# Optimization experiments

Hardware: AMD Instinct MI355X
Metric: run time of the kernel (lower is better)

The kernel has to match this reference:

```python
import jax, jax.numpy as jnp
import numpy as np

SIZE = 128
RATIO = 0.5

def setup_inputs() -> dict:
    key = jax.random.key(0)
    k1, k2, k3 = jax.random.split(key, 3)
    B, D, K = 16, 256, 18
    assp_features = jax.random.normal(k1, (B, D, SIZE, SIZE), dtype=jnp.float32)
    prototypes = jax.random.normal(k2, (B, K, D), dtype=jnp.float32)
    n_samp = int(SIZE * SIZE * RATIO)
    # sample without replacement, matching np.random.choice(replace=False)
    random_indices = jax.random.permutation(k3, SIZE * SIZE)[:n_samp].astype(jnp.int64)
    return {"assp_features": assp_features, "prototypes": prototypes,
            "random_indices": random_indices}

def reference(assp_features, prototypes, random_indices):
    # assp_features: [B, D, H, W], prototypes: [B, K, D], random_indices: [N]
    size = assp_features.shape[-1]
    x = random_indices // size  # [N]
    y = random_indices % size   # [N]
    f = assp_features[:, :, x, y]            # [B, D, N] gathered pixel features
    # squared L2 distances [B, N, K]; argmin of ||p-f||_2 == argmin of squared dist
    p2 = jnp.sum(prototypes * prototypes, axis=-1)       # [B, K]
    f2 = jnp.sum(f * f, axis=1)                          # [B, N]
    cross = jnp.einsum('bdn,bkd->bnk', f, prototypes)    # [B, N, K]
    d2 = p2[:, None, :] - 2.0 * cross + f2[:, :, None]
    idx = jnp.argmin(d2, axis=-1)                        # [B, N]
    nearest = jnp.take_along_axis(prototypes, idx[..., None], axis=1)  # [B, N, D]
    out = assp_features.at[:, :, x, y].set(jnp.swapaxes(nearest, 1, 2))
    return out
```

## Files before the change

kernel.cpp:

```cpp
#include <hip/hip_runtime.h>

constexpr int B = 16;
constexpr int D = 256;
constexpr int K = 18;
constexpr int SZ = 128;
constexpr int S = SZ * SZ;
constexpr int N = S / 2;
constexpr int PB = 512;

__global__ __launch_bounds__(256) void prep_kernel(
    const float* __restrict__ proto,
    const int* __restrict__ idx,
    unsigned char* __restrict__ mask,
    double* __restrict__ p2,
    double* __restrict__ p64,
    float* __restrict__ pT32) {
  const int blk = blockIdx.x;
  if (blk < 32) {
    mask[idx[blk * 256 + threadIdx.x]] = 1;
  } else if (blk < 104) {
    const int row  = (blk - 32) * 4 + (threadIdx.x >> 6);
    const int lane = threadIdx.x & 63;
    const float4 v = *(const float4*)(proto + (size_t)row * D + lane * 4);
    double s = (double)v.x * (double)v.x + (double)v.y * (double)v.y
             + (double)v.z * (double)v.z + (double)v.w * (double)v.w;
#pragma unroll
    for (int off = 1; off < 64; off <<= 1)
      s += __shfl_xor(s, off, 64);
    if (lane == 0) p2[row] = s;
  } else {
    const int e = (blk - 104) * 256 + threadIdx.x;
    const int b = e / (D * K);
    const int r = e - b * (D * K);
    const int d = r / K;
    const int k = r - d * K;
    const float v = proto[((size_t)b * K + k) * D + d];
    p64[e]  = (double)v;
    pT32[e] = v;
  }
}

__global__ __launch_bounds__(128, 2) void fused_kernel(
    const float* __restrict__ assp,
    const double* __restrict__ p64,
    const float* __restrict__ pT32,
    const double* __restrict__ p2,
    const unsigned char* __restrict__ mask,
    float* __restrict__ out) {
  __shared__ double spd[D * K];

  const int b     = blockIdx.x & 15;
  const int chunk = blockIdx.x >> 4;
  const int pos0  = chunk * PB;
  const int tid   = threadIdx.x;

  const double* pb = p64 + (size_t)b * D * K;
  for (int i = tid; i < D * K; i += 128) spd[i] = pb[i];
  __syncthreads();

  const float* fin = assp + (size_t)(b * D) * S + pos0 + 2 * tid;

  double acc[4][K];
#pragma unroll
  for (int jp = 0; jp < 4; ++jp)
#pragma unroll
    for (int k = 0; k < K; ++k) acc[jp][k] = 0.0;

  for (int d0 = 0; d0 < D; d0 += 8) {
    float2 fv[8][2];
#pragma unroll
    for (int jd = 0; jd < 8; ++jd) {
      fv[jd][0] = *(const float2*)(fin + (size_t)(d0 + jd) * S);
      fv[jd][1] = *(const float2*)(fin + (size_t)(d0 + jd) * S + 256);
    }
#pragma unroll
    for (int jd = 0; jd < 8; ++jd) {
      const double f0 = (double)fv[jd][0].x;
      const double f1 = (double)fv[jd][0].y;
      const double f2 = (double)fv[jd][1].x;
      const double f3 = (double)fv[jd][1].y;
      const double* pr = &spd[(d0 + jd) * K];
#pragma unroll
      for (int k = 0; k < K; ++k) {
        const double pk = pr[k];
        acc[0][k] += f0 * pk;
        acc[1][k] += f1 * pk;
        acc[2][k] += f2 * pk;
        acc[3][k] += f3 * pk;
      }
    }
  }

  const double* p2b = p2 + b * K;
  double best[4];
  int kst[4];
#pragma unroll
  for (int jp = 0; jp < 4; ++jp) { best[jp] = 1e300; kst[jp] = 0; }
#pragma unroll
  for (int k = 0; k < K; ++k) {
    const double pk2 = p2b[k];
#pragma unroll
    for (int jp = 0; jp < 4; ++jp) {
      const double d2 = pk2 - 2.0 * acc[jp][k];
      if (d2 < best[jp]) { best[jp] = d2; kst[jp] = k; }
    }
  }

  const uchar2 m0 = *(const uchar2*)(mask + pos0 + 2 * tid);
  const uchar2 m1 = *(const uchar2*)(mask + pos0 + 256 + 2 * tid);
  const float* pt = pT32 + (size_t)b * D * K;
  float* op = out + (size_t)(b * D) * S + pos0 + 2 * tid;

  for (int d0 = 0; d0 < D; d0 += 8) {
#pragma unroll
    for (int jd = 0; jd < 8; ++jd) {
      const int d = d0 + jd;
      const float2 fa = *(const float2*)(fin + (size_t)d * S);
      const float2 fb = *(const float2*)(fin + (size_t)d * S + 256);
      const float* prow = pt + d * K;
      float2 oa, ob;
      oa.x = m0.x ? prow[kst[0]] : fa.x;
      oa.y = m0.y ? prow[kst[1]] : fa.y;
      ob.x = m1.x ? prow[kst[2]] : fb.x;
      ob.y = m1.y ? prow[kst[3]] : fb.y;
      *(float2*)(op + (size_t)d * S) = oa;
      *(float2*)(op + (size_t)d * S + 256) = ob;
    }
  }
}

extern "C" void kernel_launch(void* const* d_in, const int* in_sizes, int n_in,
                              void* d_out, int out_size, void* d_ws, size_t ws_size,
                              hipStream_t stream) {
  const float* assp  = (const float*)d_in[0];
  const float* proto = (const float*)d_in[1];
  const int*   idx   = (const int*)d_in[2];
  float* out = (float*)d_out;

  unsigned char* mask = (unsigned char*)d_ws;
  double*        p2   = (double*)((char*)d_ws + S);
  double*        p64  = (double*)((char*)d_ws + S + (size_t)B * K * 8);
  float*         pT32 = (float*)((char*)p64 + (size_t)B * D * K * 8);

  hipMemsetAsync(mask, 0, S, stream);
  prep_kernel<<<392, 256, 0, stream>>>(proto, idx, mask, p2, p64, pT32);
  fused_kernel<<<B * (S / PB), 128, 0, stream>>>(assp, p64, pT32, p2, mask, out);
}
```

Measured before the change: 229.9 us.

## Drop shared-memory prototype staging, use 256 threads with two pixels each

The fused kernel no longer copies the double-precision prototypes into LDS. It reads them directly from global memory through a padded 24-double stride, so every thread loads the same row and the access is uniform. Block size doubles to 256 threads with two pixels per thread instead of four, which halves the accumulator registers. The aim is higher occupancy and removing the 36KB LDS stage and its sync. The second pass also walks d in reverse, so it likely re-reads recently cached feature rows, and it prefetches the prototype values. The cost is that all prototype reads now go through global memory and cache instead of LDS.

```diff
diff --git a/kernel.cpp b/kernel.cpp
--- a/kernel.cpp
+++ b/kernel.cpp
@@ -6,6 +6,7 @@
 constexpr int SZ = 128;
 constexpr int S = SZ * SZ;
 constexpr int N = S / 2;
+constexpr int PSTR = 24;
 constexpr int PB = 512;
 
 __global__ __launch_bounds__(256) void prep_kernel(
@@ -35,96 +36,83 @@
     const int d = r / K;
     const int k = r - d * K;
     const float v = proto[((size_t)b * K + k) * D + d];
-    p64[e]  = (double)v;
-    pT32[e] = v;
+    p64[((size_t)b * D + d) * PSTR + k] = (double)v;
+    pT32[((size_t)b * D + d) * K + k]   = v;
   }
 }
 
-__global__ __launch_bounds__(128, 2) void fused_kernel(
+__global__ __launch_bounds__(256, 2) void fused_kernel(
     const float* __restrict__ assp,
     const double* __restrict__ p64,
     const float* __restrict__ pT32,
     const double* __restrict__ p2,
     const unsigned char* __restrict__ mask,
     float* __restrict__ out) {
-  __shared__ double spd[D * K];
-
   const int b     = blockIdx.x & 15;
   const int chunk = blockIdx.x >> 4;
   const int pos0  = chunk * PB;
   const int tid   = threadIdx.x;
 
-  const double* pb = p64 + (size_t)b * D * K;
-  for (int i = tid; i < D * K; i += 128) spd[i] = pb[i];
-  __syncthreads();
+  const float*  fin = assp + (size_t)(b * D) * S + pos0 + 2 * tid;
+  const double* pb  = p64 + (size_t)b * D * PSTR;
 
-  const float* fin = assp + (size_t)(b * D) * S + pos0 + 2 * tid;
-
-  double acc[4][K];
+  double acc0[K], acc1[K];
 #pragma unroll
-  for (int jp = 0; jp < 4; ++jp)
-#pragma unroll
-    for (int k = 0; k < K; ++k) acc[jp][k] = 0.0;
+  for (int k = 0; k < K; ++k) { acc0[k] = 0.0; acc1[k] = 0.0; }
 
   for (int d0 = 0; d0 < D; d0 += 8) {
-    float2 fv[8][2];
+    float2 fv[8];
+#pragma unroll
+    for (int jd = 0; jd < 8; ++jd)
+      fv[jd] = *(const float2*)(fin + (size_t)(d0 + jd) * S);
 #pragma unroll
     for (int jd = 0; jd < 8; ++jd) {
-      fv[jd][0] = *(const float2*)(fin + (size_t)(d0 + jd) * S);
-      fv[jd][1] = *(const float2*)(fin + (size_t)(d0 + jd) * S + 256);
-    }
-#pragma unroll
-    for (int jd = 0; jd < 8; ++jd) {
-      const double f0 = (double)fv[jd][0].x;
-      const double f1 = (double)fv[jd][0].y;
-      const double f2 = (double)fv[jd][1].x;
-      const double f3 = (double)fv[jd][1].y;
-      const double* pr = &spd[(d0 + jd) * K];
+      const double f0 = (double)fv[jd].x;
+      const double f1 = (double)fv[jd].y;
+      const double* pr = pb + (size_t)(d0 + jd) * PSTR;
 #pragma unroll
       for (int k = 0; k < K; ++k) {
         const double pk = pr[k];
-        acc[0][k] += f0 * pk;
-        acc[1][k] += f1 * pk;
-        acc[2][k] += f2 * pk;
-        acc[3][k] += f3 * pk;
+        acc0[k] += f0 * pk;
+        acc1[k] += f1 * pk;
       }
     }
   }
 
   const double* p2b = p2 + b * K;
-  double best[4];
-  int kst[4];
-#pragma unroll
-  for (int jp = 0; jp < 4; ++jp) { best[jp] = 1e300; kst[jp] = 0; }
+  double best0 = 1e300, best1 = 1e300;
+  int kst0 = 0, kst1 = 0;
 #pragma unroll
   for (int k = 0; k < K; ++k) {
     const double pk2 = p2b[k];
-#pragma unroll
-    for (int jp = 0; jp < 4; ++jp) {
-      const double d2 = pk2 - 2.0 * acc[jp][k];
-      if (d2 < best[jp]) { best[jp] = d2; kst[jp] = k; }
-    }
+    const double d20 = pk2 - 2.0 * acc0[k];
+    const double d21 = pk2 - 2.0 * acc1[k];
+    if (d20 < best0) { best0 = d20; kst0 = k; }
+    if (d21 < best1) { best1 = d21; kst1 = k; }
   }
 
-  const uchar2 m0 = *(const uchar2*)(mask + pos0 + 2 * tid);
-  const uchar2 m1 = *(const uchar2*)(mask + pos0 + 256 + 2 * tid);
-  const float* pt = pT32 + (size_t)b * D * K;
+  const uchar2 m = *(const uchar2*)(mask + pos0 + 2 * tid);
+  const float* g0 = pT32 + (size_t)b * D * K + kst0;
+  const float* g1 = pT32 + (size_t)b * D * K + kst1;
   float* op = out + (size_t)(b * D) * S + pos0 + 2 * tid;
 
-  for (int d0 = 0; d0 < D; d0 += 8) {
+  for (int d0 = D - 8; d0 >= 0; d0 -= 8) {
+    float2 fa[8];
+    float  pa[8], pbv[8];
 #pragma unroll
     for (int jd = 0; jd < 8; ++jd) {
       const int d = d0 + jd;
-      const float2 fa = *(const float2*)(fin + (size_t)d * S);
-      const float2 fb = *(const float2*)(fin + (size_t)d * S + 256);
-      const float* prow = pt + d * K;
-      float2 oa, ob;
-      oa.x = m0.x ? prow[kst[0]] : fa.x;
-      oa.y = m0.y ? prow[kst[1]] : fa.y;
-      ob.x = m1.x ? prow[kst[2]] : fb.x;
-      ob.y = m1.y ? prow[kst[3]] : fb.y;
-      *(float2*)(op + (size_t)d * S) = oa;
-      *(float2*)(op + (size_t)d * S + 256) = ob;
+      fa[jd]  = *(const float2*)(fin + (size_t)d * S);
+      pa[jd]  = g0[(size_t)d * K];
+      pbv[jd] = g1[(size_t)d * K];
+    }
+#pragma unroll
+    for (int jd = 0; jd < 8; ++jd) {
+      const int d = d0 + jd;
+      float2 o;
+      o.x = m.x ? pa[jd]  : fa[jd].x;
+      o.y = m.y ? pbv[jd] : fa[jd].y;
+      *(float2*)(op + (size_t)d * S) = o;
     }
   }
 }
@@ -137,12 +125,12 @@
   const int*   idx   = (const int*)d_in[2];
   float* out = (float*)d_out;
 
-  unsigned char* mask = (unsigned char*)d_ws;
-  double*        p2   = (double*)((char*)d_ws + S);
-  double*        p64  = (double*)((char*)d_ws + S + (size_t)B * K * 8);
-  float*         pT32 = (float*)((char*)p64 + (size_t)B * D * K * 8);
+  double*        p64  = (double*)d_ws;
+  float*         pT32 = (float*)((char*)d_ws + (size_t)B * D * PSTR * 8);
+  double*        p2   = (double*)((char*)pT32 + (size_t)B * D * K * 4);
+  unsigned char* mask = (unsigned char*)((char*)p2 + (size_t)B * K * 8);
 
   hipMemsetAsync(mask, 0, S, stream);
   prep_kernel<<<392, 256, 0, stream>>>(proto, idx, mask, p2, p64, pT32);
-  fused_kernel<<<B * (S / PB), 128, 0, stream>>>(assp, p64, pT32, p2, mask, out);
+  fused_kernel<<<B * (S / PB), 256, 0, stream>>>(assp, p64, pT32, p2, mask, out);
 }
```

Result: faster. 208.9 us (-9.2%).
